# Kernel optimization log

Hardware: AMD Instinct MI355X
Metric: run time of the kernel (lower is better)

Reference implementation:

```python
import jax, jax.numpy as jnp
import numpy as np

EPS = 1e-5
K = 20
UP = 2

def _knn_idx(x, k):
    # x: (B, C, N) -> idx: (B, N, k) of nearest neighbors by squared L2
    inner = -2.0 * jnp.einsum('bcn,bcm->bnm', x, x)
    xx = jnp.sum(x * x, axis=1)  # (B, N)
    pd = -xx[:, :, None] - inner - xx[:, None, :]  # negative squared distance
    _, idx = jax.lax.top_k(pd, k)
    return idx

def _bn(x, g, b, m, v):
    # eval-mode BatchNorm2d over channel axis 1 of (B, C, N, k)
    scale = g / jnp.sqrt(v + EPS)
    return x * scale[None, :, None, None] + (b - m * scale)[None, :, None, None]

def _lrelu(x):
    return jnp.where(x >= 0, x, 0.2 * x)

def setup_inputs() -> dict:
    key = jax.random.key(0)
    ks = jax.random.split(key, 13)
    B, N, C = 16, 2048, 64
    return {
        'xyz': jax.random.normal(ks[0], (B, 3, N), dtype=jnp.float32),
        'xyz_f': jax.random.normal(ks[1], (B, C, N), dtype=jnp.float32),
        'W1': jax.random.normal(ks[2], (32, 128), dtype=jnp.float32) * 0.1,
        'g1': jax.random.uniform(ks[3], (32,), dtype=jnp.float32),
        'b1': jax.random.normal(ks[4], (32,), dtype=jnp.float32),
        'm1': jax.random.normal(ks[5], (32,), dtype=jnp.float32),
        'v1': jax.random.uniform(ks[6], (32,), dtype=jnp.float32),
        'W2': jax.random.normal(ks[7], (32, 32), dtype=jnp.float32) * 0.1,
        'g2': jax.random.uniform(ks[8], (32,), dtype=jnp.float32),
        'b2': jax.random.normal(ks[9], (32,), dtype=jnp.float32),
        'm2': jax.random.normal(ks[10], (32,), dtype=jnp.float32),
        'v2': jax.random.uniform(ks[11], (32,), dtype=jnp.float32),
        'W3': jax.random.normal(ks[12], (64, 32), dtype=jnp.float32) * 0.1,
    }

def reference(xyz, xyz_f, W1, g1, b1, m1, v1, W2, g2, b2, m2, v2, W3):
    B, C, N = xyz_f.shape
    idx = _knn_idx(xyz, K)  # (B, N, K)
    xf = jnp.transpose(xyz_f, (0, 2, 1))  # (B, N, C)
    # gather neighbor features: (B, N, K, C)
    nbr = xf[jnp.arange(B)[:, None, None], idx]
    edge = jnp.concatenate([nbr - xf[:, :, None, :],
                            jnp.broadcast_to(xf[:, :, None, :], (B, N, K, C))], axis=-1)
    f = jnp.transpose(edge, (0, 3, 1, 2))  # (B, 2C, N, K)
    f = _lrelu(_bn(jnp.einsum('oc,bcnk->bonk', W1, f), g1, b1, m1, v1))
    f = _lrelu(_bn(jnp.einsum('oc,bcnk->bonk', W2, f), g2, b2, m2, v2))
    f = jnp.einsum('oc,bcnk->bonk', W3, f)  # (B, 64, N, K)
    f = jnp.max(f, axis=-1)  # (B, 64, N)
    # point_shuffler(scale=2): (B, 64, N) -> (B, 32, 2N)
    Bc, Cc, Nc = f.shape
    f = jnp.transpose(f, (0, 2, 1)).reshape(Bc, Nc, UP, Cc // UP)
    f = f.reshape(Bc, Nc * UP, Cc // UP)
    return jnp.transpose(f, (0, 2, 1))
```

## Files before the change

### kernel.cpp

```cpp
#include <hip/hip_runtime.h>
#include <cstdint>
#include <math.h>

#define NPTS 2048
#define NBATCH 16
#define KNBR 20

#define OFF_XFT  0u
#define OFF_T1   2097152u
#define OFF_W1AF 3145728u
#define OFF_W1BF 3147776u
#define OFF_B1F  3149824u
#define OFF_W2F  3149856u
#define OFF_B2F  3150880u
#define OFF_IDX  3150912u

__global__ void fold_kernel(const float* __restrict__ W1, const float* __restrict__ g1,
                            const float* __restrict__ b1, const float* __restrict__ m1,
                            const float* __restrict__ v1, const float* __restrict__ W2,
                            const float* __restrict__ g2, const float* __restrict__ b2,
                            const float* __restrict__ m2, const float* __restrict__ v2,
                            float* __restrict__ W1AF, float* __restrict__ W1BF,
                            float* __restrict__ B1F, float* __restrict__ W2F,
                            float* __restrict__ B2F) {
  const int o = threadIdx.x;
  if (o < 32) {
    const float s1 = g1[o] / sqrtf(v1[o] + 1e-5f);
    const float s2 = g2[o] / sqrtf(v2[o] + 1e-5f);
    B1F[o] = b1[o] - m1[o] * s1;
    B2F[o] = b2[o] - m2[o] * s2;
    for (int c = 0; c < 64; ++c) {
      W1AF[o * 64 + c] = W1[o * 128 + c] * s1;
      W1BF[o * 64 + c] = W1[o * 128 + 64 + c] * s1;
    }
    for (int c = 0; c < 32; ++c) W2F[o * 32 + c] = W2[o * 32 + c] * s2;
  }
}

__global__ __launch_bounds__(256) void transpose_kernel(const float* __restrict__ in,
                                                        float* __restrict__ outT) {
  __shared__ float tile[64][65];
  const int b = blockIdx.x >> 5;
  const int n0 = (blockIdx.x & 31) << 6;
  const int tx = threadIdx.x & 63;
  const int ty = threadIdx.x >> 6;
  const float* src = in + (size_t)b * 64 * NPTS;
#pragma unroll
  for (int c = ty; c < 64; c += 4) tile[c][tx] = src[(size_t)c * NPTS + n0 + tx];
  __syncthreads();
  float* dst = outT + ((size_t)b * NPTS + n0) * 64;
#pragma unroll
  for (int nn = ty; nn < 64; nn += 4) dst[(size_t)nn * 64 + tx] = tile[tx][nn];
}

__global__ __launch_bounds__(256) void t1_kernel(const float* __restrict__ xfT,
                                                 const float* __restrict__ W1BF,
                                                 const float* __restrict__ B1F,
                                                 float* __restrict__ T1) {
  const int p = blockIdx.x * 256 + threadIdx.x;
  float acc[32];
#pragma unroll
  for (int o = 0; o < 32; ++o) acc[o] = B1F[o];
  const float* cen = xfT + (size_t)p * 64;
#pragma unroll
  for (int c0 = 0; c0 < 64; c0 += 4) {
    const float4 cv = *(const float4*)(cen + c0);
    const float cc[4] = {cv.x, cv.y, cv.z, cv.w};
#pragma unroll
    for (int o = 0; o < 32; ++o) {
#pragma unroll
      for (int j = 0; j < 4; ++j) acc[o] = fmaf(W1BF[o * 64 + c0 + j], cc[j], acc[o]);
    }
  }
  float* dst = T1 + (size_t)p * 32;
#pragma unroll
  for (int o = 0; o < 32; o += 4) {
    *(float4*)(dst + o) = make_float4(acc[o], acc[o + 1], acc[o + 2], acc[o + 3]);
  }
}

__device__ __forceinline__ float pd_of(const float4 qp, const float nqxx, const float4 c) {
  const float dot = __fadd_rn(__fadd_rn(__fmul_rn(qp.x, c.x), __fmul_rn(qp.y, c.y)),
                              __fmul_rn(qp.z, c.z));
  return __fsub_rn(__fadd_rn(nqxx, __fmul_rn(2.0f, dot)), c.w);
}

__global__ __launch_bounds__(256, 3) void knn_kernel(const float* __restrict__ xyz,
                                                     int* __restrict__ knn_out) {
  __shared__ float4 spt[NPTS];
  __shared__ int qlist[256 * KNBR];
  const int b = blockIdx.x >> 5;
  const int qbase = (blockIdx.x & 31) << 6;
  const int tid = threadIdx.x;
  const float* src = xyz + (size_t)b * 3 * NPTS;
  for (int i = tid; i < NPTS; i += 256) {
    const float x = src[i], y = src[NPTS + i], z = src[2 * NPTS + i];
    const float xx = __fadd_rn(__fadd_rn(__fmul_rn(x, x), __fmul_rn(y, y)), __fmul_rn(z, z));
    spt[i] = make_float4(x, y, z, xx);
  }
  __syncthreads();

  const int q = qbase + (tid & 63);
  const int quad = tid >> 6;
  const float4 qp = spt[q];
  const float nqxx = -qp.w;
  const int j0 = quad << 9, j1 = j0 + 512;

  float arr[KNBR];
#pragma unroll
  for (int s = 0; s < KNBR; ++s) arr[s] = -INFINITY;
  for (int j = j0; j < j1; ++j) {
    float v = pd_of(qp, nqxx, spt[j]);
#pragma unroll
    for (int s = 0; s < KNBR; ++s) {
      const float hi = fmaxf(arr[s], v);
      v = fminf(arr[s], v);
      arr[s] = hi;
    }
  }
  const float T = arr[KNBR - 1];
  int cnt = 0;
  int* myq = qlist + tid * KNBR;
  for (int j = j0; j < j1; ++j) {
    const float pd = pd_of(qp, nqxx, spt[j]);
    if (pd >= T && cnt < KNBR) { myq[cnt] = j; ++cnt; }
  }
  __syncthreads();

  if (tid < 64) {
    float bpd[KNBR];
    int bidx[KNBR];
#pragma unroll
    for (int s = 0; s < KNBR; ++s) { bpd[s] = -INFINITY; bidx[s] = 0; }
    const float4 qp2 = spt[qbase + tid];
    const float nq2 = -qp2.w;
    for (int quad2 = 0; quad2 < 4; ++quad2) {
      for (int jj = 0; jj < KNBR; ++jj) {
        const int id = qlist[((quad2 << 6) | tid) * KNBR + jj];
        const float v = pd_of(qp2, nq2, spt[id]);
        if (v > bpd[KNBR - 1]) {
#pragma unroll
          for (int s = KNBR - 1; s >= 1; --s) {
            const bool c1 = v > bpd[s - 1];
            const float pj = c1 ? bpd[s - 1] : v;
            const int ij = c1 ? bidx[s - 1] : id;
            if (v > bpd[s]) { bpd[s] = pj; bidx[s] = ij; }
          }
          if (v > bpd[0]) { bpd[0] = v; bidx[0] = id; }
        }
      }
    }
    int* dst = knn_out + ((size_t)(b * NPTS + qbase + tid)) * KNBR;
#pragma unroll
    for (int s = 0; s < KNBR; ++s) dst[s] = bidx[s];
  }
}

__global__ __launch_bounds__(256, 2) void mlp_kernel(const float* __restrict__ ws,
                                                     const int* __restrict__ knn,
                                                     const float* __restrict__ W3,
                                                     float* __restrict__ out) {
  const int t = blockIdx.x * 256 + threadIdx.x;
  const int p = t >> 2;
  const int kq = t & 3;
  const int b = p >> 11;
  const int n = p & 2047;
  const float* __restrict__ xfT = ws + OFF_XFT;
  const float* __restrict__ t1p = ws + OFF_T1 + (size_t)p * 32;
  const float* __restrict__ W1 = ws + OFF_W1AF;
  const float* __restrict__ W2 = ws + OFF_W2F;
  const float* __restrict__ B2 = ws + OFF_B2F;
  const float* __restrict__ cen = xfT + (size_t)p * 64;

  float hmax[64];
#pragma unroll
  for (int o = 0; o < 64; ++o) hmax[o] = -INFINITY;

  for (int kk = 0; kk < 5; ++kk) {
    const int k = kq * 5 + kk;
    const int nb = knn[p * KNBR + k];
    const float* __restrict__ nbr = xfT + ((size_t)(b << 11) + nb) * 64;

    float h1[32];
#pragma unroll
    for (int o = 0; o < 32; o += 4) {
      const float4 tv = *(const float4*)(t1p + o);
      h1[o] = tv.x; h1[o + 1] = tv.y; h1[o + 2] = tv.z; h1[o + 3] = tv.w;
    }
#pragma unroll
    for (int c0 = 0; c0 < 64; c0 += 8) {
      const float4 a0 = *(const float4*)(nbr + c0);
      const float4 a1 = *(const float4*)(nbr + c0 + 4);
      const float4 b0 = *(const float4*)(cen + c0);
      const float4 b1 = *(const float4*)(cen + c0 + 4);
      const float e[8] = {a0.x - b0.x, a0.y - b0.y, a0.z - b0.z, a0.w - b0.w,
                          a1.x - b1.x, a1.y - b1.y, a1.z - b1.z, a1.w - b1.w};
#pragma unroll
      for (int o = 0; o < 32; ++o) {
#pragma unroll
        for (int j = 0; j < 8; ++j) h1[o] = fmaf(W1[o * 64 + c0 + j], e[j], h1[o]);
      }
    }
#pragma unroll
    for (int o = 0; o < 32; ++o) h1[o] = fmaxf(h1[o], 0.2f * h1[o]);

    float h2[32];
#pragma unroll
    for (int o = 0; o < 32; ++o) {
      float a = B2[o];
#pragma unroll
      for (int c = 0; c < 32; ++c) a = fmaf(W2[o * 32 + c], h1[c], a);
      h2[o] = fmaxf(a, 0.2f * a);
    }
#pragma unroll
    for (int o = 0; o < 64; ++o) {
      float a = 0.f;
#pragma unroll
      for (int c = 0; c < 32; ++c) a = fmaf(W3[o * 32 + c], h2[c], a);
      hmax[o] = fmaxf(hmax[o], a);
    }
  }
#pragma unroll
  for (int o = 0; o < 64; ++o) {
    hmax[o] = fmaxf(hmax[o], __shfl_xor(hmax[o], 1));
    hmax[o] = fmaxf(hmax[o], __shfl_xor(hmax[o], 2));
  }
  if (kq == 0) {
    float* op = out + (size_t)b * (32 * 4096) + 2 * n;
#pragma unroll
    for (int f = 0; f < 64; ++f) {
      const int u = f >> 5, cc = f & 31;
      op[cc * 4096 + u] = hmax[f];
    }
  }
}

extern "C" void kernel_launch(void* const* d_in, const int* in_sizes, int n_in,
                              void* d_out, int out_size, void* d_ws, size_t ws_size,
                              hipStream_t stream) {
  const float* xyz = (const float*)d_in[0];
  const float* xyz_f = (const float*)d_in[1];
  const float* W1 = (const float*)d_in[2];
  const float* g1 = (const float*)d_in[3];
  const float* b1 = (const float*)d_in[4];
  const float* m1 = (const float*)d_in[5];
  const float* v1 = (const float*)d_in[6];
  const float* W2 = (const float*)d_in[7];
  const float* g2 = (const float*)d_in[8];
  const float* b2 = (const float*)d_in[9];
  const float* m2 = (const float*)d_in[10];
  const float* v2 = (const float*)d_in[11];
  const float* W3 = (const float*)d_in[12];
  float* ws = (float*)d_ws;
  float* out = (float*)d_out;
  int* knn = (int*)(ws + OFF_IDX);

  fold_kernel<<<1, 64, 0, stream>>>(W1, g1, b1, m1, v1, W2, g2, b2, m2, v2,
                                    ws + OFF_W1AF, ws + OFF_W1BF, ws + OFF_B1F,
                                    ws + OFF_W2F, ws + OFF_B2F);
  transpose_kernel<<<512, 256, 0, stream>>>(xyz_f, ws + OFF_XFT);
  t1_kernel<<<128, 256, 0, stream>>>(ws + OFF_XFT, ws + OFF_W1BF, ws + OFF_B1F, ws + OFF_T1);
  knn_kernel<<<512, 256, 0, stream>>>(xyz, knn);
  mlp_kernel<<<512, 256, 0, stream>>>(ws, knn, W3, out);
}
```

Baseline: 720.4 us.

## Precompute per-point W1A projection so neighbor layer-1 becomes a gather-add

Uses linearity of the first conv: W1A·(x_nbr − x_cen) + W1B·x_cen = y_nbr + (W1B·x_cen − W1A·x_cen + bias), with y = W1A·x precomputed once per point. A new pre-kernel computes y and the per-point constant term directly from the untransposed input, replacing both the transpose and the t1 kernels. The MLP kernel then gathers 32 floats per neighbor instead of running a 64x32 matvec per edge, which removes most of its layer-1 FLOPs and halves the gathered bytes. The pre-kernel reads channels with a stride of NPTS but coalesced across threads, and the change in summation order alters rounding slightly.

Result: faster. 640.1 us (-11.2%).

```diff
diff --git a/kernel.cpp b/kernel.cpp
--- a/kernel.cpp
+++ b/kernel.cpp
@@ -6,14 +6,13 @@
 #define NBATCH 16
 #define KNBR 20
 
-#define OFF_XFT  0u
-#define OFF_T1   2097152u
-#define OFF_W1AF 3145728u
-#define OFF_W1BF 3147776u
-#define OFF_B1F  3149824u
-#define OFF_W2F  3149856u
-#define OFF_B2F  3150880u
-#define OFF_IDX  3150912u
+#define OFF_YT   0u
+#define OFF_W1AF 2097152u
+#define OFF_W1BF 2099200u
+#define OFF_B1F  2101248u
+#define OFF_W2F  2101280u
+#define OFF_B2F  2102304u
+#define OFF_IDX  2102336u
 
 __global__ void fold_kernel(const float* __restrict__ W1, const float* __restrict__ g1,
                             const float* __restrict__ b1, const float* __restrict__ m1,
@@ -37,45 +36,35 @@
   }
 }
 
-__global__ __launch_bounds__(256) void transpose_kernel(const float* __restrict__ in,
-                                                        float* __restrict__ outT) {
-  __shared__ float tile[64][65];
-  const int b = blockIdx.x >> 5;
-  const int n0 = (blockIdx.x & 31) << 6;
-  const int tx = threadIdx.x & 63;
-  const int ty = threadIdx.x >> 6;
-  const float* src = in + (size_t)b * 64 * NPTS;
-#pragma unroll
-  for (int c = ty; c < 64; c += 4) tile[c][tx] = src[(size_t)c * NPTS + n0 + tx];
-  __syncthreads();
-  float* dst = outT + ((size_t)b * NPTS + n0) * 64;
-#pragma unroll
-  for (int nn = ty; nn < 64; nn += 4) dst[(size_t)nn * 64 + tx] = tile[tx][nn];
-}
-
-__global__ __launch_bounds__(256) void t1_kernel(const float* __restrict__ xfT,
-                                                 const float* __restrict__ W1BF,
-                                                 const float* __restrict__ B1F,
-                                                 float* __restrict__ T1) {
+__global__ __launch_bounds__(256) void pre_kernel(const float* __restrict__ xf,
+                                                  const float* __restrict__ W1AF,
+                                                  const float* __restrict__ W1BF,
+                                                  const float* __restrict__ B1F,
+                                                  float* __restrict__ yt) {
   const int p = blockIdx.x * 256 + threadIdx.x;
-  float acc[32];
-#pragma unroll
-  for (int o = 0; o < 32; ++o) acc[o] = B1F[o];
-  const float* cen = xfT + (size_t)p * 64;
-#pragma unroll
-  for (int c0 = 0; c0 < 64; c0 += 4) {
-    const float4 cv = *(const float4*)(cen + c0);
-    const float cc[4] = {cv.x, cv.y, cv.z, cv.w};
-#pragma unroll
-    for (int o = 0; o < 32; ++o) {
-#pragma unroll
-      for (int j = 0; j < 4; ++j) acc[o] = fmaf(W1BF[o * 64 + c0 + j], cc[j], acc[o]);
-    }
-  }
-  float* dst = T1 + (size_t)p * 32;
+  const int b = p >> 11, n = p & 2047;
+  const float* src = xf + (size_t)b * 64 * NPTS + n;
+  float cen[64];
+#pragma unroll
+  for (int c = 0; c < 64; ++c) cen[c] = src[(size_t)c * NPTS];
+  float y[32], t1[32];
+#pragma unroll
+  for (int o = 0; o < 32; ++o) {
+    float a = 0.f;
+    float bb = B1F[o];
+#pragma unroll
+    for (int c = 0; c < 64; ++c) {
+      a = fmaf(W1AF[o * 64 + c], cen[c], a);
+      bb = fmaf(W1BF[o * 64 + c], cen[c], bb);
+    }
+    y[o] = a;
+    t1[o] = bb - a;
+  }
+  float* dst = yt + (size_t)p * 64;
 #pragma unroll
   for (int o = 0; o < 32; o += 4) {
-    *(float4*)(dst + o) = make_float4(acc[o], acc[o + 1], acc[o + 2], acc[o + 3]);
+    *(float4*)(dst + o) = make_float4(y[o], y[o + 1], y[o + 2], y[o + 3]);
+    *(float4*)(dst + 32 + o) = make_float4(t1[o], t1[o + 1], t1[o + 2], t1[o + 3]);
   }
 }
 
@@ -165,41 +154,37 @@
   const int kq = t & 3;
   const int b = p >> 11;
   const int n = p & 2047;
-  const float* __restrict__ xfT = ws + OFF_XFT;
-  const float* __restrict__ t1p = ws + OFF_T1 + (size_t)p * 32;
-  const float* __restrict__ W1 = ws + OFF_W1AF;
+  const float* __restrict__ yt = ws + OFF_YT;
   const float* __restrict__ W2 = ws + OFF_W2F;
   const float* __restrict__ B2 = ws + OFF_B2F;
-  const float* __restrict__ cen = xfT + (size_t)p * 64;
-
+  const float* __restrict__ ybase = yt + ((size_t)(b << 11)) * 64;
+
+  float t1c[32];
+  {
+    const float* tp = yt + (size_t)p * 64 + 32;
+#pragma unroll
+    for (int o = 0; o < 32; o += 4) {
+      const float4 v = *(const float4*)(tp + o);
+      t1c[o] = v.x; t1c[o + 1] = v.y; t1c[o + 2] = v.z; t1c[o + 3] = v.w;
+    }
+  }
   float hmax[64];
 #pragma unroll
   for (int o = 0; o < 64; ++o) hmax[o] = -INFINITY;
 
+#pragma unroll 1
   for (int kk = 0; kk < 5; ++kk) {
-    const int k = kq * 5 + kk;
-    const int nb = knn[p * KNBR + k];
-    const float* __restrict__ nbr = xfT + ((size_t)(b << 11) + nb) * 64;
+    const int nb = knn[p * KNBR + kq * 5 + kk] & 2047;
+    const float* __restrict__ yp = ybase + (size_t)nb * 64;
 
     float h1[32];
 #pragma unroll
     for (int o = 0; o < 32; o += 4) {
-      const float4 tv = *(const float4*)(t1p + o);
-      h1[o] = tv.x; h1[o + 1] = tv.y; h1[o + 2] = tv.z; h1[o + 3] = tv.w;
-    }
-#pragma unroll
-    for (int c0 = 0; c0 < 64; c0 += 8) {
-      const float4 a0 = *(const float4*)(nbr + c0);
-      const float4 a1 = *(const float4*)(nbr + c0 + 4);
-      const float4 b0 = *(const float4*)(cen + c0);
-      const float4 b1 = *(const float4*)(cen + c0 + 4);
-      const float e[8] = {a0.x - b0.x, a0.y - b0.y, a0.z - b0.z, a0.w - b0.w,
-                          a1.x - b1.x, a1.y - b1.y, a1.z - b1.z, a1.w - b1.w};
-#pragma unroll
-      for (int o = 0; o < 32; ++o) {
-#pragma unroll
-        for (int j = 0; j < 8; ++j) h1[o] = fmaf(W1[o * 64 + c0 + j], e[j], h1[o]);
-      }
+      const float4 v = *(const float4*)(yp + o);
+      h1[o] = t1c[o] + v.x;
+      h1[o + 1] = t1c[o + 1] + v.y;
+      h1[o + 2] = t1c[o + 2] + v.z;
+      h1[o + 3] = t1c[o + 3] + v.w;
     }
 #pragma unroll
     for (int o = 0; o < 32; ++o) h1[o] = fmaxf(h1[o], 0.2f * h1[o]);
@@ -258,8 +243,8 @@
   fold_kernel<<<1, 64, 0, stream>>>(W1, g1, b1, m1, v1, W2, g2, b2, m2, v2,
                                     ws + OFF_W1AF, ws + OFF_W1BF, ws + OFF_B1F,
                                     ws + OFF_W2F, ws + OFF_B2F);
-  transpose_kernel<<<512, 256, 0, stream>>>(xyz_f, ws + OFF_XFT);
-  t1_kernel<<<128, 256, 0, stream>>>(ws + OFF_XFT, ws + OFF_W1BF, ws + OFF_B1F, ws + OFF_T1);
+  pre_kernel<<<128, 256, 0, stream>>>(xyz_f, ws + OFF_W1AF, ws + OFF_W1BF, ws + OFF_B1F,
+                                      ws + OFF_YT);
   knn_kernel<<<512, 256, 0, stream>>>(xyz, knn);
   mlp_kernel<<<512, 256, 0, stream>>>(ws, knn, W3, out);
 }
```
